# Kernel tuning notes

Measured on AMD Instinct MI355X. Metric: run time of the kernel, lower is better.

The kernel has to match this reference:

```python
import jax, jax.numpy as jnp
import numpy as np

N_GAUSSIANS = 512
N_PIXELS = 262144  # 512x512 image


def setup_inputs() -> dict:
    key = jax.random.key(0)
    k1, k2, k3, k4, k5 = jax.random.split(key, 5)
    x = jax.random.uniform(k1, (N_PIXELS, 2), dtype=jnp.float32)
    alphas = (1.0 / N_GAUSSIANS) ** 0.5 * jax.random.uniform(k2, (N_GAUSSIANS, 1), dtype=jnp.float32)
    means = jax.random.uniform(k3, (N_GAUSSIANS, 2), dtype=jnp.float32)
    rotations = jnp.pi * jax.random.uniform(k4, (N_GAUSSIANS, 1), dtype=jnp.float32)
    scales = 0.1 * jax.random.uniform(k5, (N_GAUSSIANS, 2), dtype=jnp.float32)
    return {"x": x, "alphas": alphas, "means": means, "rotations": rotations, "scales": scales}


def _inv2x2(m):
    # m: [N, 2, 2] -> elementwise 2x2 inverse
    a, b = m[:, 0, 0], m[:, 0, 1]
    c, d = m[:, 1, 0], m[:, 1, 1]
    det = a * d - b * c
    inv = jnp.stack([jnp.stack([d, -b], axis=-1),
                     jnp.stack([-c, a], axis=-1)], axis=-2)
    return inv / det[:, None, None]


def reference(x, alphas, means, rotations, scales):
    rot = rotations[:, 0]                       # [N]
    cth, sth = jnp.cos(rot), jnp.sin(rot)
    s0, s1 = scales[:, 0], scales[:, 1]
    # RS = R @ diag(s): [N, 2, 2]
    RS = jnp.stack([s0 * cth, -s1 * sth, s0 * sth, s1 * cth], axis=-1).reshape(-1, 2, 2)
    RSSR = jnp.einsum('nij,nkj->nik', RS, RS)   # RS @ RS^T
    cov = _inv2x2(RSSR)                          # [N, 2, 2]
    rel = x[:, None, :] - means[None, :, :]      # [P, N, 2]
    q = jnp.einsum('pni,nij,pnj->pn', rel, cov, rel)  # quadratic form [P, N]
    g = jnp.exp(-q / 2)                          # [P, N]
    return g @ alphas                            # [P, 1]
```

## Files before the change

kernel.cpp:

```cpp
#include <hip/hip_runtime.h>

#define NG 512
#define NPX 262144
#define BLOCK 256
#define PXPT 2

#if __has_builtin(__builtin_amdgcn_exp2f)
  #define KSCALE 0.72134752044448170368f
  #define EXPNEG(w) __builtin_amdgcn_exp2f(-(w))
#else
  #define KSCALE 0.5f
  #define EXPNEG(w) __expf(-(w))
#endif

__global__ __launch_bounds__(BLOCK, 2)
void gsplat_kernel(const float* __restrict__ x,
                   const float* __restrict__ alphas,
                   const float* __restrict__ means,
                   const float* __restrict__ rotations,
                   const float* __restrict__ scales,
                   float* __restrict__ out)
{
    __shared__ float4 ga[NG];
    __shared__ float2 gb[NG];

    for (int n = threadIdx.x; n < NG; n += BLOCK) {
        float rot = rotations[n];
        float sth, cth;
        sincosf(rot, &sth, &cth);
        float s0 = scales[2 * n + 0];
        float s1 = scales[2 * n + 1];
        float r00 = s0 * cth, r01 = -s1 * sth;
        float r10 = s0 * sth, r11 =  s1 * cth;
        float Ar = r00 * r00 + r01 * r01;
        float Br = r00 * r10 + r01 * r11;
        float Dr = r10 * r10 + r11 * r11;
        float det = Ar * Dr - Br * Br;
        float kc00 =  KSCALE * Dr / det;
        float kc01 = -KSCALE * Br / det;
        float p00 = sqrtf(kc00);
        float p01 = kc01 / p00;
        float p11 = sqrtf(KSCALE / Dr);
        float mx = means[2 * n + 0];
        float my = means[2 * n + 1];
        float nuoff = -(p00 * mx + p01 * my);
        float nvoff = -(p11 * my);
        ga[n] = make_float4(p00, p01, nuoff, alphas[n]);
        gb[n] = make_float2(p11, nvoff);
    }
    __syncthreads();

    int tid = blockIdx.x * BLOCK + threadIdx.x;
    float4 xv = ((const float4*)x)[tid];
    float x0 = xv.x, y0 = xv.y;
    float x1 = xv.z, y1 = xv.w;

    float acc0 = 0.0f, acc1 = 0.0f;
    #pragma unroll 16
    for (int n = 0; n < NG; ++n) {
        float4 a = ga[n];
        float2 b = gb[n];
        float u0 = fmaf(a.x, x0, fmaf(a.y, y0, a.z));
        float v0 = fmaf(b.x, y0, b.y);
        float u1 = fmaf(a.x, x1, fmaf(a.y, y1, a.z));
        float v1 = fmaf(b.x, y1, b.y);
        float w0 = fmaf(v0, v0, u0 * u0);
        float w1 = fmaf(v1, v1, u1 * u1);
        acc0 = fmaf(a.w, EXPNEG(w0), acc0);
        acc1 = fmaf(a.w, EXPNEG(w1), acc1);
    }

    ((float2*)out)[tid] = make_float2(acc0, acc1);
}

extern "C" void kernel_launch(void* const* d_in, const int* in_sizes, int n_in,
                              void* d_out, int out_size, void* d_ws, size_t ws_size,
                              hipStream_t stream) {
    const float* x         = (const float*)d_in[0];
    const float* alphas    = (const float*)d_in[1];
    const float* means     = (const float*)d_in[2];
    const float* rotations = (const float*)d_in[3];
    const float* scales    = (const float*)d_in[4];
    float* out = (float*)d_out;

    int grid = NPX / (BLOCK * PXPT);
    gsplat_kernel<<<grid, BLOCK, 0, stream>>>(x, alphas, means, rotations, scales, out);
}
```

Measured before the change: 98.56 us.

## Switch to one pixel per thread with tiled gaussian register batches

Each thread now handles a single pixel instead of two, the grid doubles, and gaussian parameters are loaded from LDS in batches of eight into registers before being evaluated with two alternating accumulators. Launch bounds are raised to target more waves per SIMD. This trades per-thread ILP and LDS data reuse (each LDS read now serves one pixel) for higher occupancy, and doubles the per-block gaussian setup work.

Measured after the change: 91.84 us. 1.07x faster.

```diff
diff --git a/kernel.cpp b/kernel.cpp
--- a/kernel.cpp
+++ b/kernel.cpp
@@ -3,7 +3,7 @@
 #define NG 512
 #define NPX 262144
 #define BLOCK 256
-#define PXPT 2
+#define GTILE 8
 
 #if __has_builtin(__builtin_amdgcn_exp2f)
   #define KSCALE 0.72134752044448170368f
@@ -13,7 +13,7 @@
   #define EXPNEG(w) __expf(-(w))
 #endif
 
-__global__ __launch_bounds__(BLOCK, 2)
+__global__ __launch_bounds__(BLOCK, 4)
 void gsplat_kernel(const float* __restrict__ x,
                    const float* __restrict__ alphas,
                    const float* __restrict__ means,
@@ -51,26 +51,30 @@
     __syncthreads();
 
     int tid = blockIdx.x * BLOCK + threadIdx.x;
-    float4 xv = ((const float4*)x)[tid];
+    float2 xv = ((const float2*)x)[tid];
     float x0 = xv.x, y0 = xv.y;
-    float x1 = xv.z, y1 = xv.w;
 
     float acc0 = 0.0f, acc1 = 0.0f;
-    #pragma unroll 16
-    for (int n = 0; n < NG; ++n) {
-        float4 a = ga[n];
-        float2 b = gb[n];
-        float u0 = fmaf(a.x, x0, fmaf(a.y, y0, a.z));
-        float v0 = fmaf(b.x, y0, b.y);
-        float u1 = fmaf(a.x, x1, fmaf(a.y, y1, a.z));
-        float v1 = fmaf(b.x, y1, b.y);
-        float w0 = fmaf(v0, v0, u0 * u0);
-        float w1 = fmaf(v1, v1, u1 * u1);
-        acc0 = fmaf(a.w, EXPNEG(w0), acc0);
-        acc1 = fmaf(a.w, EXPNEG(w1), acc1);
+    for (int t = 0; t < NG; t += GTILE) {
+        float4 a[GTILE];
+        float2 b[GTILE];
+        #pragma unroll
+        for (int j = 0; j < GTILE; ++j) {
+            a[j] = ga[t + j];
+            b[j] = gb[t + j];
+        }
+        #pragma unroll
+        for (int j = 0; j < GTILE; ++j) {
+            float u = fmaf(a[j].x, x0, fmaf(a[j].y, y0, a[j].z));
+            float v = fmaf(b[j].x, y0, b[j].y);
+            float w = fmaf(v, v, u * u);
+            float e = EXPNEG(w);
+            if (j & 1) acc1 = fmaf(a[j].w, e, acc1);
+            else       acc0 = fmaf(a[j].w, e, acc0);
+        }
     }
 
-    ((float2*)out)[tid] = make_float2(acc0, acc1);
+    out[tid] = acc0 + acc1;
 }
 
 extern "C" void kernel_launch(void* const* d_in, const int* in_sizes, int n_in,
@@ -83,6 +87,6 @@
     const float* scales    = (const float*)d_in[4];
     float* out = (float*)d_out;
 
-    int grid = NPX / (BLOCK * PXPT);
+    int grid = NPX / BLOCK;
     gsplat_kernel<<<grid, BLOCK, 0, stream>>>(x, alphas, means, rotations, scales, out);
 }
```
